# Kernel optimization log

Measured on AMD Instinct MI355X. Metric: run time of the kernel, lower is better.

The kernel has to match this reference:

```python
import jax, jax.numpy as jnp
import numpy as np

IN_F, HID, OUT, NN = 64, 128, 64, 128
TOTAL = 4096  # 32 graphs * 128 nodes


def setup_inputs() -> dict:
    key = jax.random.key(0)
    ks = jax.random.split(key, 8)
    d_in = 1 + 2 * IN_F
    s1 = 1.0 / np.sqrt(d_in)
    s2 = 1.0 / np.sqrt(HID)
    return {
        "feat": jax.random.normal(ks[0], (TOTAL, IN_F), jnp.float32),
        "coordinate": jax.random.normal(ks[1], (TOTAL, 3), jnp.float32),
        "W1": jax.random.uniform(ks[2], (d_in, HID), jnp.float32, -s1, s1),
        "b1": jax.random.uniform(ks[3], (HID,), jnp.float32, -s1, s1),
        "W2": jax.random.uniform(ks[4], (HID, HID), jnp.float32, -s2, s2),
        "b2": jax.random.uniform(ks[5], (HID,), jnp.float32, -s2, s2),
        "W3": jax.random.uniform(ks[6], (HID, OUT), jnp.float32, -s2, s2),
        "b3": jax.random.uniform(ks[7], (OUT,), jnp.float32, -s2, s2),
        "num_nodes": NN,
    }


def reference(feat, coordinate, W1, b1, W2, b2, W3, b3, num_nodes):
    N = num_nodes
    B = feat.shape[0] // N
    h = feat.reshape(B, N, -1)        # [B,N,F]
    x = coordinate.reshape(B, N, -1)  # [B,N,3]
    # pairwise squared distance: [B,N,N,1]
    d2 = jnp.sum((x[:, None, :, :] - x[:, :, None, :]) ** 2, axis=-1, keepdims=True)
    F = h.shape[-1]
    # feat concat order matches torch: [h_j broadcast over dim1, h_i broadcast over dim2]
    hj = jnp.broadcast_to(h[:, None, :, :], (B, N, N, F))
    hi = jnp.broadcast_to(h[:, :, None, :], (B, N, N, F))
    z = jnp.concatenate([d2, hj, hi], axis=-1)  # [B,N,N,1+2F]
    z = jax.nn.silu(z @ W1 + b1)
    z = jax.nn.silu(z @ W2 + b2)
    z = z @ W3 + b3                   # [B,N,N,OUT]
    return jnp.sum(z, axis=(1, 2))    # [B,OUT]
```

## Files before the change

### kernel.cpp

```cpp
#include <hip/hip_runtime.h>
#include <hip/hip_bf16.h>

#define F_IN 64
#define HID 128
#define OUTF 64
#define NN 128
#define NB 32
#define TOTAL 4096

typedef short bf16x8 __attribute__((ext_vector_type(8)));
typedef float f32x4 __attribute__((ext_vector_type(4)));

static __device__ __forceinline__ short f2bf(float v) {
  __hip_bfloat16 h = __float2bfloat16(v);
  return __builtin_bit_cast(short, h);
}
static __device__ __forceinline__ float fast_silu(float v) {
  return v * __builtin_amdgcn_rcpf(1.f + __expf(-v));
}

__global__ __launch_bounds__(256) void uv_prep(
    const float* __restrict__ feat,
    const float* __restrict__ W1,
    const float* __restrict__ W2,
    const float* __restrict__ b1,
    float* __restrict__ uv,
    __hip_bfloat16* __restrict__ w2swz) {
  __shared__ __align__(16) char wcat[256 * 128];
  const int tid = threadIdx.x;

  {
    const int c = tid;
    const int cc = c & 127;
    const int rbase = (c < HID) ? 1 : 65;
#pragma unroll
    for (int p = 0; p < 8; ++p) {
      bf16x8 pk;
#pragma unroll
      for (int m = 0; m < 8; ++m)
        pk[m] = f2bf(W1[(rbase + p * 8 + m) * HID + cc]);
      *reinterpret_cast<bf16x8*>(wcat + c * 128 + ((p ^ (c & 7)) << 4)) = pk;
    }
  }
  if (blockIdx.x < 64) {
    const int e = blockIdx.x * 256 + tid;
    const int kk = e >> 7, cc2 = e & 127;
    const int byo = cc2 * 256 + (((kk >> 3) ^ (cc2 & 7)) << 4) + (kk & 7) * 2;
    *reinterpret_cast<__hip_bfloat16*>(reinterpret_cast<char*>(w2swz) + byo) =
        __float2bfloat16(W2[kk * HID + cc2]);
  }
  __syncthreads();

  const int wave = tid >> 6, lane = tid & 63;
  const int lr = lane & 15, kg = lane >> 4;
  const int r0 = blockIdx.x * 16;

  f32x4 acc[4];
#pragma unroll
  for (int ct = 0; ct < 4; ++ct) acc[ct] = {0.f, 0.f, 0.f, 0.f};

#pragma unroll
  for (int ks = 0; ks < 2; ++ks) {
    const float* fp = feat + (size_t)(r0 + lr) * F_IN + ks * 32 + kg * 8;
    const f32x4 fa = *reinterpret_cast<const f32x4*>(fp);
    const f32x4 fb = *reinterpret_cast<const f32x4*>(fp + 4);
    bf16x8 a;
#pragma unroll
    for (int m = 0; m < 4; ++m) {
      a[m] = f2bf(fa[m]);
      a[4 + m] = f2bf(fb[m]);
    }
    const int slot = ks * 4 + kg;
#pragma unroll
    for (int ct = 0; ct < 4; ++ct) {
      const int c = wave * 64 + ct * 16 + lr;
      const bf16x8 w = *reinterpret_cast<const bf16x8*>(
          wcat + c * 128 + ((slot ^ (c & 7)) << 4));
      acc[ct] = __builtin_amdgcn_mfma_f32_16x16x32_bf16(a, w, acc[ct], 0, 0, 0);
    }
  }
#pragma unroll
  for (int ct = 0; ct < 4; ++ct) {
    const int c = wave * 64 + ct * 16 + lr;
    const float badd = (c >= HID) ? b1[c - HID] : 0.f;
#pragma unroll
    for (int reg = 0; reg < 4; ++reg) {
      const int r = r0 + kg * 4 + reg;
      uv[(size_t)r * 256 + c] = acc[ct][reg] + badd;
    }
  }
}

__global__ __launch_bounds__(512, 2) void sake_main(
    const float* __restrict__ coord,
    const float* __restrict__ W1,
    const float* __restrict__ b2,
    const float* __restrict__ uv,
    const __hip_bfloat16* __restrict__ w2swz,
    float* __restrict__ part) {
  __shared__ __align__(16) char w2lds[HID * 256];
  __shared__ float ssum[8][HID];

  const int tid = threadIdx.x;
  const int bid = (blockIdx.x & 7) * 128 + (blockIdx.x >> 3);
  const int b = bid >> 5;
  const int ig = bid & 31;

#pragma unroll
  for (int p = 0; p < 4; ++p) {
    const int o = (tid + p * 512) * 16;
    *reinterpret_cast<int4*>(w2lds + o) =
        *reinterpret_cast<const int4*>(reinterpret_cast<const char*>(w2swz) + o);
  }

  const int wave = tid >> 6, lane = tid & 63;
  const int lr = lane & 15, kg = lane >> 4;
  const int i = ig * 4 + (wave >> 1);
  const int j0 = (wave & 1) * 64;

  const float* xi = coord + (size_t)(b * NN + i) * 3;
  const float xix = xi[0], xiy = xi[1], xiz = xi[2];
  float d2t[4];
#pragma unroll
  for (int t = 0; t < 4; ++t) {
    const float* xj = coord + (size_t)(b * NN + j0 + t * 16 + lr) * 3;
    const float dx = xj[0] - xix, dy = xj[1] - xiy, dz = xj[2] - xiz;
    d2t[t] = dx * dx + dy * dy + dz * dz;
  }

  f32x4 acc[4][8];
#pragma unroll
  for (int ct = 0; ct < 8; ++ct) {
    const float bb = b2[ct * 16 + lr];
#pragma unroll
    for (int t = 0; t < 4; ++t) acc[t][ct] = {bb, bb, bb, bb};
  }

  const float* vrow = uv + ((size_t)b * NN + i) * 256 + HID;
  const float* urow0 = uv + ((size_t)b * NN + j0 + lr) * 256;

  __syncthreads();

#pragma unroll
  for (int ks = 0; ks < 4; ++ks) {
    const int c0 = ks * 32 + kg * 8;
    bf16x8 wf[8];
    const int rbase = lr * 256 + ((((ks << 2) | kg) ^ (lr & 7)) << 4);
#pragma unroll
    for (int ct = 0; ct < 8; ++ct)
      wf[ct] = *reinterpret_cast<const bf16x8*>(w2lds + rbase + ct * 4096);

    const f32x4 va = *reinterpret_cast<const f32x4*>(vrow + c0);
    const f32x4 vb = *reinterpret_cast<const f32x4*>(vrow + c0 + 4);
    const f32x4 wa = *reinterpret_cast<const f32x4*>(W1 + c0);
    const f32x4 wb = *reinterpret_cast<const f32x4*>(W1 + c0 + 4);

#pragma unroll
    for (int t = 0; t < 4; ++t) {
      const float* up = urow0 + t * 4096 + c0;
      const f32x4 ua = *reinterpret_cast<const f32x4*>(up);
      const f32x4 ub = *reinterpret_cast<const f32x4*>(up + 4);
      bf16x8 a;
#pragma unroll
      for (int m = 0; m < 4; ++m) {
        a[m] = f2bf(fast_silu(fmaf(d2t[t], wa[m], ua[m] + va[m])));
        a[4 + m] = f2bf(fast_silu(fmaf(d2t[t], wb[m], ub[m] + vb[m])));
      }
#pragma unroll
      for (int ct = 0; ct < 8; ++ct)
        acc[t][ct] = __builtin_amdgcn_mfma_f32_16x16x32_bf16(a, wf[ct],
                                                             acc[t][ct], 0, 0, 0);
    }
  }

  float csum[8];
#pragma unroll
  for (int ct = 0; ct < 8; ++ct) {
    float s = 0.f;
#pragma unroll
    for (int t = 0; t < 4; ++t)
#pragma unroll
      for (int reg = 0; reg < 4; ++reg) {
        const float v = acc[t][ct][reg];
        s = fmaf(v, __builtin_amdgcn_rcpf(1.f + __expf(-v)), s);
      }
    s += __shfl_xor(s, 16);
    s += __shfl_xor(s, 32);
    csum[ct] = s;
  }
  if (lane < 16) {
#pragma unroll
    for (int ct = 0; ct < 8; ++ct) ssum[wave][ct * 16 + lane] = csum[ct];
  }
  __syncthreads();
  if (tid < HID) {
    float s = 0.f;
#pragma unroll
    for (int w = 0; w < 8; ++w) s += ssum[w][tid];
    part[(size_t)bid * HID + tid] = s;
  }
}

__global__ void final_kernel(const float* __restrict__ part,
                             const float* __restrict__ W3,
                             const float* __restrict__ b3,
                             float* __restrict__ out) {
  __shared__ float s2[2][HID];
  __shared__ float s[HID];
  int b = blockIdx.x, t = threadIdx.x;
  int c = t & 127, half = t >> 7;
  float a = 0.f;
  for (int g = half * 16; g < half * 16 + 16; ++g)
    a += part[(size_t)(b * 32 + g) * HID + c];
  s2[half][c] = a;
  __syncthreads();
  if (t < HID) s[t] = s2[0][t] + s2[1][t];
  __syncthreads();
  if (t < OUTF) {
    float o = 16384.f * b3[t];
    for (int c2 = 0; c2 < HID; ++c2) o += s[c2] * W3[c2 * OUTF + t];
    out[b * OUTF + t] = o;
  }
}

extern "C" void kernel_launch(void* const* d_in, const int* in_sizes, int n_in,
                              void* d_out, int out_size, void* d_ws, size_t ws_size,
                              hipStream_t stream) {
  const float* feat = (const float*)d_in[0];
  const float* coord = (const float*)d_in[1];
  const float* W1 = (const float*)d_in[2];
  const float* b1 = (const float*)d_in[3];
  const float* W2 = (const float*)d_in[4];
  const float* b2 = (const float*)d_in[5];
  const float* W3 = (const float*)d_in[6];
  const float* b3 = (const float*)d_in[7];
  float* out = (float*)d_out;

  char* ws = (char*)d_ws;
  __hip_bfloat16* w2swz = (__hip_bfloat16*)ws;
  float* uv = (float*)(ws + 64 * 1024);
  float* part = (float*)(ws + 64 * 1024 + 4096 * 1024);

  uv_prep<<<256, 256, 0, stream>>>(feat, W1, W2, b1, uv, w2swz);
  sake_main<<<1024, 512, 0, stream>>>(coord, W1, b2, uv, w2swz, part);
  final_kernel<<<NB, 256, 0, stream>>>(part, W3, b3, out);
}
```

Before: 68.82 us.

## Halve per-block work in main kernel and use packed Newton-reciprocal SiLU

```diff
diff --git a/kernel.cpp b/kernel.cpp
--- a/kernel.cpp
+++ b/kernel.cpp
@@ -10,13 +10,24 @@
 
 typedef short bf16x8 __attribute__((ext_vector_type(8)));
 typedef float f32x4 __attribute__((ext_vector_type(4)));
+typedef float f32x2 __attribute__((ext_vector_type(2)));
+typedef unsigned int u32x2 __attribute__((ext_vector_type(2)));
 
 static __device__ __forceinline__ short f2bf(float v) {
   __hip_bfloat16 h = __float2bfloat16(v);
   return __builtin_bit_cast(short, h);
 }
-static __device__ __forceinline__ float fast_silu(float v) {
-  return v * __builtin_amdgcn_rcpf(1.f + __expf(-v));
+
+static __device__ __forceinline__ f32x2 silu2(f32x2 v) {
+  f32x2 e;
+  e.x = fminf(__expf(-v.x), 1e13f);
+  e.y = fminf(__expf(-v.y), 1e13f);
+  f32x2 x = e + 1.f;
+  u32x2 yi = (u32x2)(0x7EF311C3u) - __builtin_bit_cast(u32x2, x);
+  f32x2 y = __builtin_bit_cast(f32x2, yi);
+  y = y * (2.f - x * y);
+  y = y * (2.f - x * y);
+  return v * y;
 }
 
 __global__ __launch_bounds__(256) void uv_prep(
@@ -28,7 +39,6 @@
     __hip_bfloat16* __restrict__ w2swz) {
   __shared__ __align__(16) char wcat[256 * 128];
   const int tid = threadIdx.x;
-
   {
     const int c = tid;
     const int cc = c & 127;
@@ -102,9 +112,9 @@
   __shared__ float ssum[8][HID];
 
   const int tid = threadIdx.x;
-  const int bid = (blockIdx.x & 7) * 128 + (blockIdx.x >> 3);
-  const int b = bid >> 5;
-  const int ig = bid & 31;
+  const int bid = (blockIdx.x & 7) * 256 + (blockIdx.x >> 3);
+  const int b = bid >> 6;
+  const int i0 = (bid & 63) * 2;
 
 #pragma unroll
   for (int p = 0; p < 4; ++p) {
@@ -115,25 +125,25 @@
 
   const int wave = tid >> 6, lane = tid & 63;
   const int lr = lane & 15, kg = lane >> 4;
-  const int i = ig * 4 + (wave >> 1);
-  const int j0 = (wave & 1) * 64;
+  const int i = i0 + (wave >> 2);
+  const int j0 = (wave & 3) * 32;
 
   const float* xi = coord + (size_t)(b * NN + i) * 3;
   const float xix = xi[0], xiy = xi[1], xiz = xi[2];
-  float d2t[4];
-#pragma unroll
-  for (int t = 0; t < 4; ++t) {
+  float d2t[2];
+#pragma unroll
+  for (int t = 0; t < 2; ++t) {
     const float* xj = coord + (size_t)(b * NN + j0 + t * 16 + lr) * 3;
     const float dx = xj[0] - xix, dy = xj[1] - xiy, dz = xj[2] - xiz;
     d2t[t] = dx * dx + dy * dy + dz * dz;
   }
 
-  f32x4 acc[4][8];
+  f32x4 acc[2][8];
 #pragma unroll
   for (int ct = 0; ct < 8; ++ct) {
     const float bb = b2[ct * 16 + lr];
 #pragma unroll
-    for (int t = 0; t < 4; ++t) acc[t][ct] = {bb, bb, bb, bb};
+    for (int t = 0; t < 2; ++t) acc[t][ct] = {bb, bb, bb, bb};
   }
 
   const float* vrow = uv + ((size_t)b * NN + i) * 256 + HID;
@@ -154,17 +164,33 @@
     const f32x4 vb = *reinterpret_cast<const f32x4*>(vrow + c0 + 4);
     const f32x4 wa = *reinterpret_cast<const f32x4*>(W1 + c0);
     const f32x4 wb = *reinterpret_cast<const f32x4*>(W1 + c0 + 4);
-
-#pragma unroll
-    for (int t = 0; t < 4; ++t) {
+    f32x2 vp2[4] = {__builtin_shufflevector(va, va, 0, 1),
+                    __builtin_shufflevector(va, va, 2, 3),
+                    __builtin_shufflevector(vb, vb, 0, 1),
+                    __builtin_shufflevector(vb, vb, 2, 3)};
+    f32x2 wp2[4] = {__builtin_shufflevector(wa, wa, 0, 1),
+                    __builtin_shufflevector(wa, wa, 2, 3),
+                    __builtin_shufflevector(wb, wb, 0, 1),
+                    __builtin_shufflevector(wb, wb, 2, 3)};
+
+#pragma unroll
+    for (int t = 0; t < 2; ++t) {
       const float* up = urow0 + t * 4096 + c0;
       const f32x4 ua = *reinterpret_cast<const f32x4*>(up);
       const f32x4 ub = *reinterpret_cast<const f32x4*>(up + 4);
+      f32x2 up2[4] = {__builtin_shufflevector(ua, ua, 0, 1),
+                      __builtin_shufflevector(ua, ua, 2, 3),
+                      __builtin_shufflevector(ub, ub, 0, 1),
+                      __builtin_shufflevector(ub, ub, 2, 3)};
+      const f32x2 d2v = {d2t[t], d2t[t]};
       bf16x8 a;
 #pragma unroll
-      for (int m = 0; m < 4; ++m) {
-        a[m] = f2bf(fast_silu(fmaf(d2t[t], wa[m], ua[m] + va[m])));
-        a[4 + m] = f2bf(fast_silu(fmaf(d2t[t], wb[m], ub[m] + vb[m])));
+      for (int p = 0; p < 4; ++p) {
+        f32x2 z = up2[p] + vp2[p];
+        z = d2v * wp2[p] + z;
+        const f32x2 s = silu2(z);
+        a[2 * p] = f2bf(s.x);
+        a[2 * p + 1] = f2bf(s.y);
       }
 #pragma unroll
       for (int ct = 0; ct < 8; ++ct)
@@ -176,14 +202,14 @@
   float csum[8];
 #pragma unroll
   for (int ct = 0; ct < 8; ++ct) {
-    float s = 0.f;
-#pragma unroll
-    for (int t = 0; t < 4; ++t)
-#pragma unroll
-      for (int reg = 0; reg < 4; ++reg) {
-        const float v = acc[t][ct][reg];
-        s = fmaf(v, __builtin_amdgcn_rcpf(1.f + __expf(-v)), s);
-      }
+    f32x2 sp = {0.f, 0.f};
+#pragma unroll
+    for (int t = 0; t < 2; ++t) {
+      const f32x4 av = acc[t][ct];
+      sp += silu2(__builtin_shufflevector(av, av, 0, 1));
+      sp += silu2(__builtin_shufflevector(av, av, 2, 3));
+    }
+    float s = sp.x + sp.y;
     s += __shfl_xor(s, 16);
     s += __shfl_xor(s, 32);
     csum[ct] = s;
@@ -210,8 +236,8 @@
   int b = blockIdx.x, t = threadIdx.x;
   int c = t & 127, half = t >> 7;
   float a = 0.f;
-  for (int g = half * 16; g < half * 16 + 16; ++g)
-    a += part[(size_t)(b * 32 + g) * HID + c];
+  for (int g = half * 32; g < half * 32 + 32; ++g)
+    a += part[(size_t)(b * 64 + g) * HID + c];
   s2[half][c] = a;
   __syncthreads();
   if (t < HID) s[t] = s2[0][t] + s2[1][t];
@@ -242,6 +268,6 @@
   float* part = (float*)(ws + 64 * 1024 + 4096 * 1024);
 
   uv_prep<<<256, 256, 0, stream>>>(feat, W1, W2, b1, uv, w2swz);
-  sake_main<<<1024, 512, 0, stream>>>(coord, W1, b2, uv, w2swz, part);
+  sake_main<<<2048, 512, 0, stream>>>(coord, W1, b2, uv, w2swz, part);
   final_kernel<<<NB, 256, 0, stream>>>(part, W3, b3, out);
 }
```

After: 81.48 us. 1.18x slower.

## Split main kernel into one-row 256-thread blocks and prescale for exp2 SiLU

Applied to the files above, without the earlier changes.

```diff
diff --git a/kernel.cpp b/kernel.cpp
--- a/kernel.cpp
+++ b/kernel.cpp
@@ -8,6 +8,9 @@
 #define NB 32
 #define TOTAL 4096
 
+#define NEG_LOG2E (-1.4426950408889634f)
+#define NEG_LN2 (-0.6931471805599453f)
+
 typedef short bf16x8 __attribute__((ext_vector_type(8)));
 typedef float f32x4 __attribute__((ext_vector_type(4)));
 
@@ -15,8 +18,13 @@
   __hip_bfloat16 h = __float2bfloat16(v);
   return __builtin_bit_cast(short, h);
 }
-static __device__ __forceinline__ float fast_silu(float v) {
-  return v * __builtin_amdgcn_rcpf(1.f + __expf(-v));
+
+static __device__ __forceinline__ float fexp2(float x) {
+#if __has_builtin(__builtin_amdgcn_exp2f)
+  return __builtin_amdgcn_exp2f(x);
+#else
+  return exp2f(x);
+#endif
 }
 
 __global__ __launch_bounds__(256) void uv_prep(
@@ -24,11 +32,13 @@
     const float* __restrict__ W1,
     const float* __restrict__ W2,
     const float* __restrict__ b1,
-    float* __restrict__ uv,
-    __hip_bfloat16* __restrict__ w2swz) {
+    const float* __restrict__ b2,
+    float* __restrict__ uvp,
+    __hip_bfloat16* __restrict__ w2swz,
+    float* __restrict__ w0p,
+    float* __restrict__ b2p) {
   __shared__ __align__(16) char wcat[256 * 128];
   const int tid = threadIdx.x;
-
   {
     const int c = tid;
     const int cc = c & 127;
@@ -48,6 +58,9 @@
     const int byo = cc2 * 256 + (((kk >> 3) ^ (cc2 & 7)) << 4) + (kk & 7) * 2;
     *reinterpret_cast<__hip_bfloat16*>(reinterpret_cast<char*>(w2swz) + byo) =
         __float2bfloat16(W2[kk * HID + cc2]);
+  } else if (blockIdx.x == 64) {
+    if (tid < HID) w0p[tid] = NEG_LOG2E * W1[tid];
+    else b2p[tid - HID] = NEG_LOG2E * b2[tid - HID];
   }
   __syncthreads();
 
@@ -86,118 +99,124 @@
 #pragma unroll
     for (int reg = 0; reg < 4; ++reg) {
       const int r = r0 + kg * 4 + reg;
-      uv[(size_t)r * 256 + c] = acc[ct][reg] + badd;
-    }
-  }
-}
-
-__global__ __launch_bounds__(512, 2) void sake_main(
+      uvp[(size_t)r * 256 + c] = NEG_LOG2E * (acc[ct][reg] + badd);
+    }
+  }
+}
+
+__global__ __launch_bounds__(256, 4) void sake_main(
     const float* __restrict__ coord,
-    const float* __restrict__ W1,
-    const float* __restrict__ b2,
-    const float* __restrict__ uv,
+    const float* __restrict__ w0p,
+    const float* __restrict__ b2p,
+    const float* __restrict__ uvp,
     const __hip_bfloat16* __restrict__ w2swz,
     float* __restrict__ part) {
   __shared__ __align__(16) char w2lds[HID * 256];
-  __shared__ float ssum[8][HID];
+  __shared__ float ssum[4][HID];
 
   const int tid = threadIdx.x;
-  const int bid = (blockIdx.x & 7) * 128 + (blockIdx.x >> 3);
-  const int b = bid >> 5;
-  const int ig = bid & 31;
-
-#pragma unroll
-  for (int p = 0; p < 4; ++p) {
-    const int o = (tid + p * 512) * 16;
-    *reinterpret_cast<int4*>(w2lds + o) =
-        *reinterpret_cast<const int4*>(reinterpret_cast<const char*>(w2swz) + o);
+  const int bid = (blockIdx.x & 7) * 512 + (blockIdx.x >> 3);
+  const int b = bid >> 7, i = bid & 127;
+
+  {
+    const char* src = reinterpret_cast<const char*>(w2swz);
+#pragma unroll
+    for (int p = 0; p < 8; ++p) {
+      const int o = tid * 16 + p * 4096;
+      *reinterpret_cast<int4*>(w2lds + o) =
+          *reinterpret_cast<const int4*>(src + o);
+    }
   }
 
   const int wave = tid >> 6, lane = tid & 63;
   const int lr = lane & 15, kg = lane >> 4;
-  const int i = ig * 4 + (wave >> 1);
-  const int j0 = (wave & 1) * 64;
+  const int j0 = wave * 32;
 
   const float* xi = coord + (size_t)(b * NN + i) * 3;
   const float xix = xi[0], xiy = xi[1], xiz = xi[2];
-  float d2t[4];
-#pragma unroll
-  for (int t = 0; t < 4; ++t) {
+  float d2t[2];
+#pragma unroll
+  for (int t = 0; t < 2; ++t) {
     const float* xj = coord + (size_t)(b * NN + j0 + t * 16 + lr) * 3;
     const float dx = xj[0] - xix, dy = xj[1] - xiy, dz = xj[2] - xiz;
     d2t[t] = dx * dx + dy * dy + dz * dz;
   }
 
-  f32x4 acc[4][8];
-#pragma unroll
-  for (int ct = 0; ct < 8; ++ct) {
-    const float bb = b2[ct * 16 + lr];
-#pragma unroll
-    for (int t = 0; t < 4; ++t) acc[t][ct] = {bb, bb, bb, bb};
-  }
-
-  const float* vrow = uv + ((size_t)b * NN + i) * 256 + HID;
-  const float* urow0 = uv + ((size_t)b * NN + j0 + lr) * 256;
+  f32x4 acc[2][8];
+#pragma unroll
+  for (int c = 0; c < 8; ++c) {
+    const float bb = b2p[c * 16 + lr];
+    acc[0][c] = {bb, bb, bb, bb};
+    acc[1][c] = {bb, bb, bb, bb};
+  }
+
+  const float* vrow = uvp + ((size_t)b * NN + i) * 256 + HID;
+  const float* u0 = uvp + ((size_t)b * NN + j0 + lr) * 256;
+  const float* u1 = u0 + 16 * 256;
 
   __syncthreads();
 
 #pragma unroll
   for (int ks = 0; ks < 4; ++ks) {
     const int c0 = ks * 32 + kg * 8;
-    bf16x8 wf[8];
+    bf16x8 zb[2];
+#pragma unroll
+    for (int t = 0; t < 2; ++t) {
+      const float* up = (t ? u1 : u0) + c0;
+#pragma unroll
+      for (int h = 0; h < 2; ++h) {
+        const f32x4 u4 = *reinterpret_cast<const f32x4*>(up + h * 4);
+        const f32x4 v4 = *reinterpret_cast<const f32x4*>(vrow + c0 + h * 4);
+        const f32x4 w4 = *reinterpret_cast<const f32x4*>(w0p + c0 + h * 4);
+#pragma unroll
+        for (int m = 0; m < 4; ++m) {
+          const float z = fmaf(d2t[t], w4[m], u4[m] + v4[m]);
+          zb[t][h * 4 + m] = f2bf(z * __builtin_amdgcn_rcpf(1.f + fexp2(z)));
+        }
+      }
+    }
     const int rbase = lr * 256 + ((((ks << 2) | kg) ^ (lr & 7)) << 4);
-#pragma unroll
-    for (int ct = 0; ct < 8; ++ct)
-      wf[ct] = *reinterpret_cast<const bf16x8*>(w2lds + rbase + ct * 4096);
-
-    const f32x4 va = *reinterpret_cast<const f32x4*>(vrow + c0);
-    const f32x4 vb = *reinterpret_cast<const f32x4*>(vrow + c0 + 4);
-    const f32x4 wa = *reinterpret_cast<const f32x4*>(W1 + c0);
-    const f32x4 wb = *reinterpret_cast<const f32x4*>(W1 + c0 + 4);
-
-#pragma unroll
-    for (int t = 0; t < 4; ++t) {
-      const float* up = urow0 + t * 4096 + c0;
-      const f32x4 ua = *reinterpret_cast<const f32x4*>(up);
-      const f32x4 ub = *reinterpret_cast<const f32x4*>(up + 4);
-      bf16x8 a;
+    bf16x8 wf[4];
+#pragma unroll
+    for (int c = 0; c < 4; ++c)
+      wf[c] = *reinterpret_cast<const bf16x8*>(w2lds + rbase + c * 4096);
+#pragma unroll
+    for (int c = 0; c < 4; ++c) {
+      acc[0][c] = __builtin_amdgcn_mfma_f32_16x16x32_bf16(zb[0], wf[c], acc[0][c], 0, 0, 0);
+      acc[1][c] = __builtin_amdgcn_mfma_f32_16x16x32_bf16(zb[1], wf[c], acc[1][c], 0, 0, 0);
+    }
+#pragma unroll
+    for (int c = 0; c < 4; ++c)
+      wf[c] = *reinterpret_cast<const bf16x8*>(w2lds + rbase + (4 + c) * 4096);
+#pragma unroll
+    for (int c = 0; c < 4; ++c) {
+      acc[0][4 + c] = __builtin_amdgcn_mfma_f32_16x16x32_bf16(zb[0], wf[c], acc[0][4 + c], 0, 0, 0);
+      acc[1][4 + c] = __builtin_amdgcn_mfma_f32_16x16x32_bf16(zb[1], wf[c], acc[1][4 + c], 0, 0, 0);
+    }
+  }
+
+#pragma unroll
+  for (int c = 0; c < 8; ++c) {
+    float s = 0.f;
+#pragma unroll
+    for (int t = 0; t < 2; ++t)
 #pragma unroll
       for (int m = 0; m < 4; ++m) {
-        a[m] = f2bf(fast_silu(fmaf(d2t[t], wa[m], ua[m] + va[m])));
-        a[4 + m] = f2bf(fast_silu(fmaf(d2t[t], wb[m], ub[m] + vb[m])));
-      }
-#pragma unroll
-      for (int ct = 0; ct < 8; ++ct)
-        acc[t][ct] = __builtin_amdgcn_mfma_f32_16x16x32_bf16(a, wf[ct],
-                                                             acc[t][ct], 0, 0, 0);
-    }
-  }
-
-  float csum[8];
-#pragma unroll
-  for (int ct = 0; ct < 8; ++ct) {
-    float s = 0.f;
-#pragma unroll
-    for (int t = 0; t < 4; ++t)
-#pragma unroll
-      for (int reg = 0; reg < 4; ++reg) {
-        const float v = acc[t][ct][reg];
-        s = fmaf(v, __builtin_amdgcn_rcpf(1.f + __expf(-v)), s);
+        const float z = acc[t][c][m];
+        s = fmaf(z, __builtin_amdgcn_rcpf(1.f + fexp2(z)), s);
       }
     s += __shfl_xor(s, 16);
     s += __shfl_xor(s, 32);
-    csum[ct] = s;
+    acc[0][c][0] = s;
   }
   if (lane < 16) {
 #pragma unroll
-    for (int ct = 0; ct < 8; ++ct) ssum[wave][ct * 16 + lane] = csum[ct];
+    for (int c = 0; c < 8; ++c) ssum[wave][c * 16 + lane] = acc[0][c][0];
   }
   __syncthreads();
   if (tid < HID) {
-    float s = 0.f;
-#pragma unroll
-    for (int w = 0; w < 8; ++w) s += ssum[w][tid];
-    part[(size_t)bid * HID + tid] = s;
+    part[(size_t)bid * HID + tid] =
+        ssum[0][tid] + ssum[1][tid] + ssum[2][tid] + ssum[3][tid];
   }
 }
 
@@ -210,11 +229,11 @@
   int b = blockIdx.x, t = threadIdx.x;
   int c = t & 127, half = t >> 7;
   float a = 0.f;
-  for (int g = half * 16; g < half * 16 + 16; ++g)
-    a += part[(size_t)(b * 32 + g) * HID + c];
+  for (int g = half * 64; g < half * 64 + 64; ++g)
+    a += part[(size_t)(b * NN + g) * HID + c];
   s2[half][c] = a;
   __syncthreads();
-  if (t < HID) s[t] = s2[0][t] + s2[1][t];
+  if (t < HID) s[t] = (s2[0][t] + s2[1][t]) * NEG_LN2;
   __syncthreads();
   if (t < OUTF) {
     float o = 16384.f * b3[t];
@@ -238,10 +257,12 @@
 
   char* ws = (char*)d_ws;
   __hip_bfloat16* w2swz = (__hip_bfloat16*)ws;
-  float* uv = (float*)(ws + 64 * 1024);
+  float* w0p = (float*)(ws + 32 * 1024);
+  float* b2p = (float*)(ws + 36 * 1024);
+  float* uvp = (float*)(ws + 64 * 1024);
   float* part = (float*)(ws + 64 * 1024 + 4096 * 1024);
 
-  uv_prep<<<256, 256, 0, stream>>>(feat, W1, W2, b1, uv, w2swz);
-  sake_main<<<1024, 512, 0, stream>>>(coord, W1, b2, uv, w2swz, part);
+  uv_prep<<<256, 256, 0, stream>>>(feat, W1, W2, b1, b2, uvp, w2swz, w0p, b2p);
+  sake_main<<<TOTAL, 256, 0, stream>>>(coord, w0p, b2p, uvp, w2swz, part);
   final_kernel<<<NB, 256, 0, stream>>>(part, W3, b3, out);
 }
```

New measurement: 60.48 us. 1.14x faster.
